# Kernel optimization log

Hardware: AMD Instinct MI355X
Metric: run time of the kernel (lower is better)

Reference implementation:

```python
import jax, jax.numpy as jnp
import numpy as np

NODE_DIM = 128
EDGE_ATTR_DIM = 64
OUT_DIM = 128
N_NODES = 10000
N_EDGES = 640000


def setup_inputs() -> dict:
    key = jax.random.key(0)
    k1, k2, k3, k4, k5, k6, k7 = jax.random.split(key, 7)
    x = jax.random.normal(k1, (N_NODES, NODE_DIM), dtype=jnp.float32)
    edge_index = jax.random.randint(k2, (2, N_EDGES), 0, N_NODES, dtype=jnp.int64)
    edge_attr = jax.random.normal(k3, (N_EDGES, EDGE_ATTR_DIM), dtype=jnp.float32)
    in_dim = 2 * NODE_DIM + EDGE_ATTR_DIM  # 320
    s1 = 1.0 / np.sqrt(in_dim)
    s2 = 1.0 / np.sqrt(OUT_DIM)
    W1 = jax.random.uniform(k4, (in_dim, OUT_DIM), jnp.float32, -s1, s1)
    b1 = jax.random.uniform(k5, (OUT_DIM,), jnp.float32, -s1, s1)
    W2 = jax.random.uniform(k6, (OUT_DIM, OUT_DIM), jnp.float32, -s2, s2)
    b2 = jax.random.uniform(k7, (OUT_DIM,), jnp.float32, -s2, s2)
    return {"x": x, "edge_index": edge_index, "edge_attr": edge_attr,
            "W1": W1, "b1": b1, "W2": W2, "b2": b2}


def reference(x, edge_index, edge_attr, W1, b1, W2, b2):
    src, tgt = edge_index[0], edge_index[1]
    x_i = x[src]                      # [E, node_dim] gather
    x_j = x[tgt]                      # [E, node_dim] gather
    edge_input = jnp.concatenate([x_i, x_j, edge_attr], axis=1)  # [E, 320]
    h = jax.nn.relu(edge_input @ W1 + b1)   # [E, out_dim]
    return h @ W2 + b2                      # [E, out_dim]
```

## Files before the change

### kernel.cpp

```cpp
#include <hip/hip_runtime.h>


typedef __bf16 bf16;
typedef __attribute__((ext_vector_type(8)))  __bf16 bf16x8;
typedef __attribute__((ext_vector_type(4)))  __bf16 bf16x4;
typedef __attribute__((ext_vector_type(16))) float  f32x16;

#define N_EDGES 640000
#define BM      256
#define NTHR    512

__global__ void prep_weights(const float* __restrict__ W1, const float* __restrict__ W2,
                             bf16* __restrict__ w1f, bf16* __restrict__ w2f) {
    int i = blockIdx.x * 256 + threadIdx.x;
    if (i < 40960) {
        int j = i & 7, l = (i >> 3) & 63, q = i >> 9;
        int ks = q % 20, nt = q / 20;
        int n = nt * 32 + (l & 31);
        int k = ks * 16 + ((l >> 5) << 3) + j;
        w1f[i] = (bf16)W1[k * 128 + n];
    } else if (i < 40960 + 16384) {
        int i2 = i - 40960;
        int j = i2 & 7, l = (i2 >> 3) & 63, q = i2 >> 9;
        int ks = q & 7, nt = q >> 3;
        int n = nt * 32 + (l & 31);
        int k = ks * 16 + ((l >> 5) << 3) + j;
        w2f[i2] = (bf16)W2[k * 128 + n];
    }
}

__device__ __forceinline__ void write_h(const f32x16& a, int mt, int nt, int ln, int rowq,
                                        bf16* sA, const float* sB1) {
    const int n    = nt * 32 + ln;
    const float bi = sB1[n];
    const int base = ((mt * 8 + (n >> 4)) * 64 + ((n >> 3) & 1) * 32) * 8 + (n & 7);
#pragma unroll
    for (int r = 0; r < 16; ++r) {
        const int ml = (r & 3) + ((r >> 2) << 3) + rowq;
        float v = a[r] + bi;
        sA[base + ml * 8] = (bf16)fmaxf(v, 0.f);
    }
}

__device__ __forceinline__ void write_out(const f32x16& a, int mt, int nt, int ln, int rowq,
                                          int ebase, const float* sB2, float* out) {
    const int n    = nt * 32 + ln;
    const float bi = sB2[n];
#pragma unroll
    for (int r = 0; r < 16; ++r) {
        const int ml = (r & 3) + ((r >> 2) << 3) + rowq;
        const size_t off = (size_t)(ebase + mt * 32 + ml) * 128 + n;
        __builtin_nontemporal_store(a[r] + bi, &out[off]);
    }
}

#define G1_STEP(KL, KS) {                                                          \
    bf16x8 a0  = *(const bf16x8*)&sA[((mt0 * 8 + (KL)) * 64 + lane) * 8];          \
    bf16x8 a1  = *(const bf16x8*)&sA[(((mt0 + 1) * 8 + (KL)) * 64 + lane) * 8];    \
    bf16x8 bb0 = *(const bf16x8*)&sW[((nt0 * 20 + (KS)) * 64 + lane) * 8];         \
    bf16x8 bb1 = *(const bf16x8*)&sW[(((nt0 + 1) * 20 + (KS)) * 64 + lane) * 8];   \
    acc00 = __builtin_amdgcn_mfma_f32_32x32x16_bf16(a0, bb0, acc00, 0, 0, 0);      \
    acc01 = __builtin_amdgcn_mfma_f32_32x32x16_bf16(a0, bb1, acc01, 0, 0, 0);      \
    acc10 = __builtin_amdgcn_mfma_f32_32x32x16_bf16(a1, bb0, acc10, 0, 0, 0);      \
    acc11 = __builtin_amdgcn_mfma_f32_32x32x16_bf16(a1, bb1, acc11, 0, 0, 0); }

#define G2_STEP(KS) {                                                              \
    bf16x8 a0  = *(const bf16x8*)&sA[((mt0 * 8 + (KS)) * 64 + lane) * 8];          \
    bf16x8 a1  = *(const bf16x8*)&sA[(((mt0 + 1) * 8 + (KS)) * 64 + lane) * 8];    \
    bf16x8 bb0 = *(const bf16x8*)&sW[((nt0 * 8 + (KS)) * 64 + lane) * 8];          \
    bf16x8 bb1 = *(const bf16x8*)&sW[(((nt0 + 1) * 8 + (KS)) * 64 + lane) * 8];    \
    acc00 = __builtin_amdgcn_mfma_f32_32x32x16_bf16(a0, bb0, acc00, 0, 0, 0);      \
    acc01 = __builtin_amdgcn_mfma_f32_32x32x16_bf16(a0, bb1, acc01, 0, 0, 0);      \
    acc10 = __builtin_amdgcn_mfma_f32_32x32x16_bf16(a1, bb0, acc10, 0, 0, 0);      \
    acc11 = __builtin_amdgcn_mfma_f32_32x32x16_bf16(a1, bb1, acc11, 0, 0, 0); }

__global__ __launch_bounds__(NTHR, 2) void edge_mlp(
    const float* __restrict__ x, const int* __restrict__ eidx,
    const float* __restrict__ eattr, const bf16* __restrict__ w1f,
    const float* __restrict__ b1, const bf16* __restrict__ w2f,
    const float* __restrict__ b2, float* __restrict__ out)
{
    extern __shared__ char smem[];
    bf16*  sW   = (bf16*)smem;
    bf16*  sA   = (bf16*)(smem + 81920);
    int*   sSrc = (int*)(smem + 81920 + 65536);
    int*   sTgt = sSrc + 256;
    float* sB1  = (float*)(sTgt + 256);
    float* sB2  = sB1 + 128;

    const int tid   = threadIdx.x;
    const int wave  = tid >> 6;
    const int lane  = tid & 63;
    const int ebase = blockIdx.x * BM;

    if (tid < BM) sSrc[tid] = eidx[ebase + tid];
    else          sTgt[tid - BM] = eidx[N_EDGES + ebase + (tid - BM)];
    if (tid < 128)        sB1[tid] = b1[tid];
    if (tid >= NTHR - 128) sB2[tid - (NTHR - 128)] = b2[tid - (NTHR - 128)];
    {
        const uint4* s4 = (const uint4*)w1f;
        uint4*       d4 = (uint4*)sW;
#pragma unroll
        for (int i = 0; i < 10; ++i) d4[i * NTHR + tid] = s4[i * NTHR + tid];
    }

    const int mt0 = (wave >> 1) * 2;
    const int nt0 = (wave & 1) * 2;

    f32x16 acc00, acc01, acc10, acc11;
#pragma unroll
    for (int i = 0; i < 16; ++i) { acc00[i] = 0.f; acc01[i] = 0.f; acc10[i] = 0.f; acc11[i] = 0.f; }

    const int m_st   = tid >> 1;
    const int ch     = (tid & 1) << 6;
    const int mt8_st = (m_st >> 5) * 8;
    const int ml_st  = m_st & 31;

#pragma unroll
    for (int p = 0; p < 2; ++p) {
        __syncthreads();
        {
            const int row = (p == 0) ? sSrc[m_st] : sTgt[m_st];
            const float4* xr = (const float4*)(x + (size_t)row * 128);
#pragma unroll
            for (int i = 0; i < 16; ++i) {
                const int c = ch + i * 4;
                float4 v = xr[c >> 2];
                bf16x4 bv; bv[0] = (bf16)v.x; bv[1] = (bf16)v.y; bv[2] = (bf16)v.z; bv[3] = (bf16)v.w;
                *((bf16x4*)&sA[((mt8_st + (c >> 4)) * 64 + ml_st + ((c >> 3) & 1) * 32) * 8 + (c & 7)]) = bv;
            }
        }
        __syncthreads();
#pragma unroll
        for (int kl = 0; kl < 8; ++kl) G1_STEP(kl, p * 8 + kl);
    }

    __syncthreads();
    {
#pragma unroll
        for (int i = 0; i < 8; ++i) {
            const int p4 = tid + i * NTHR;
            const int m  = p4 >> 4;
            const int c  = (p4 & 15) << 2;
            float4 v = ((const float4*)eattr)[(size_t)(ebase + m) * 16 + (p4 & 15)];
            bf16x4 bv; bv[0] = (bf16)v.x; bv[1] = (bf16)v.y; bv[2] = (bf16)v.z; bv[3] = (bf16)v.w;
            *((bf16x4*)&sA[(((m >> 5) * 8 + (c >> 4)) * 64 + (m & 31) + ((c >> 3) & 1) * 32) * 8 + (c & 7)]) = bv;
        }
    }
    __syncthreads();
#pragma unroll
    for (int kl = 0; kl < 4; ++kl) G1_STEP(kl, 16 + kl);

    __syncthreads();
    {
        const uint4* s4 = (const uint4*)w2f;
        uint4*       d4 = (uint4*)sW;
#pragma unroll
        for (int i = 0; i < 4; ++i) d4[i * NTHR + tid] = s4[i * NTHR + tid];
    }
    {
        const int rowq = (lane >> 5) * 4;
        const int ln   = lane & 31;
        write_h(acc00, mt0,     nt0,     ln, rowq, sA, sB1);
        write_h(acc01, mt0,     nt0 + 1, ln, rowq, sA, sB1);
        write_h(acc10, mt0 + 1, nt0,     ln, rowq, sA, sB1);
        write_h(acc11, mt0 + 1, nt0 + 1, ln, rowq, sA, sB1);
    }
    __syncthreads();

#pragma unroll
    for (int i = 0; i < 16; ++i) { acc00[i] = 0.f; acc01[i] = 0.f; acc10[i] = 0.f; acc11[i] = 0.f; }
#pragma unroll
    for (int ks = 0; ks < 8; ++ks) G2_STEP(ks);

    {
        const int rowq = (lane >> 5) * 4;
        const int ln   = lane & 31;
        write_out(acc00, mt0,     nt0,     ln, rowq, ebase, sB2, out);
        write_out(acc01, mt0,     nt0 + 1, ln, rowq, ebase, sB2, out);
        write_out(acc10, mt0 + 1, nt0,     ln, rowq, ebase, sB2, out);
        write_out(acc11, mt0 + 1, nt0 + 1, ln, rowq, ebase, sB2, out);
    }
}

extern "C" void kernel_launch(void* const* d_in, const int* in_sizes, int n_in,
                              void* d_out, int out_size, void* d_ws, size_t ws_size,
                              hipStream_t stream) {
    const float* x   = (const float*)d_in[0];
    const int*   ei  = (const int*)d_in[1];
    const float* ea  = (const float*)d_in[2];
    const float* W1  = (const float*)d_in[3];
    const float* b1  = (const float*)d_in[4];
    const float* W2  = (const float*)d_in[5];
    const float* b2  = (const float*)d_in[6];
    float*       out = (float*)d_out;

    bf16* w1f = (bf16*)d_ws;
    bf16* w2f = (bf16*)((char*)d_ws + 81920);

    prep_weights<<<224, 256, 0, stream>>>(W1, W2, w1f, w2f);

    const size_t shmem = 150528;
    edge_mlp<<<N_EDGES / BM, NTHR, shmem, stream>>>(x, ei, ea, w1f, b1, w2f, b2, out);
}
```

Measured before the change: 576.8 us.

## Shrink edge tile, keep weights in registers, swizzle hidden-layer LDS

Cuts the block tile from 256 to 64 edges with 256 threads, so LDS use drops from about 147KB to 56KB and more blocks fit per CU. Each wave now loads its own W1/W2 column slice straight into registers instead of staging the full weights in LDS, and the whole 320-wide gathered input is staged in one pass with no intermediate barriers. The hidden activations go to a separate XOR-swizzled LDS buffer to avoid bank conflicts, and setprio is raised around the MFMA loops. The cost is that every block reloads the weights from global memory/L2 (four times as many blocks) and holds more registers per thread.

After: 620.6 us. 7.6% more time.

```diff
diff --git a/kernel.cpp b/kernel.cpp
--- a/kernel.cpp
+++ b/kernel.cpp
@@ -3,12 +3,12 @@
 
 typedef __bf16 bf16;
 typedef __attribute__((ext_vector_type(8)))  __bf16 bf16x8;
-typedef __attribute__((ext_vector_type(4)))  __bf16 bf16x4;
+typedef __attribute__((ext_vector_type(4)))  float  f32x4;
 typedef __attribute__((ext_vector_type(16))) float  f32x16;
 
 #define N_EDGES 640000
-#define BM      256
-#define NTHR    512
+#define BM      64
+#define NTHR    256
 
 __global__ void prep_weights(const float* __restrict__ W1, const float* __restrict__ W2,
                              bf16* __restrict__ w1f, bf16* __restrict__ w2f) {
@@ -29,51 +29,6 @@
     }
 }
 
-__device__ __forceinline__ void write_h(const f32x16& a, int mt, int nt, int ln, int rowq,
-                                        bf16* sA, const float* sB1) {
-    const int n    = nt * 32 + ln;
-    const float bi = sB1[n];
-    const int base = ((mt * 8 + (n >> 4)) * 64 + ((n >> 3) & 1) * 32) * 8 + (n & 7);
-#pragma unroll
-    for (int r = 0; r < 16; ++r) {
-        const int ml = (r & 3) + ((r >> 2) << 3) + rowq;
-        float v = a[r] + bi;
-        sA[base + ml * 8] = (bf16)fmaxf(v, 0.f);
-    }
-}
-
-__device__ __forceinline__ void write_out(const f32x16& a, int mt, int nt, int ln, int rowq,
-                                          int ebase, const float* sB2, float* out) {
-    const int n    = nt * 32 + ln;
-    const float bi = sB2[n];
-#pragma unroll
-    for (int r = 0; r < 16; ++r) {
-        const int ml = (r & 3) + ((r >> 2) << 3) + rowq;
-        const size_t off = (size_t)(ebase + mt * 32 + ml) * 128 + n;
-        __builtin_nontemporal_store(a[r] + bi, &out[off]);
-    }
-}
-
-#define G1_STEP(KL, KS) {                                                          \
-    bf16x8 a0  = *(const bf16x8*)&sA[((mt0 * 8 + (KL)) * 64 + lane) * 8];          \
-    bf16x8 a1  = *(const bf16x8*)&sA[(((mt0 + 1) * 8 + (KL)) * 64 + lane) * 8];    \
-    bf16x8 bb0 = *(const bf16x8*)&sW[((nt0 * 20 + (KS)) * 64 + lane) * 8];         \
-    bf16x8 bb1 = *(const bf16x8*)&sW[(((nt0 + 1) * 20 + (KS)) * 64 + lane) * 8];   \
-    acc00 = __builtin_amdgcn_mfma_f32_32x32x16_bf16(a0, bb0, acc00, 0, 0, 0);      \
-    acc01 = __builtin_amdgcn_mfma_f32_32x32x16_bf16(a0, bb1, acc01, 0, 0, 0);      \
-    acc10 = __builtin_amdgcn_mfma_f32_32x32x16_bf16(a1, bb0, acc10, 0, 0, 0);      \
-    acc11 = __builtin_amdgcn_mfma_f32_32x32x16_bf16(a1, bb1, acc11, 0, 0, 0); }
-
-#define G2_STEP(KS) {                                                              \
-    bf16x8 a0  = *(const bf16x8*)&sA[((mt0 * 8 + (KS)) * 64 + lane) * 8];          \
-    bf16x8 a1  = *(const bf16x8*)&sA[(((mt0 + 1) * 8 + (KS)) * 64 + lane) * 8];    \
-    bf16x8 bb0 = *(const bf16x8*)&sW[((nt0 * 8 + (KS)) * 64 + lane) * 8];          \
-    bf16x8 bb1 = *(const bf16x8*)&sW[(((nt0 + 1) * 8 + (KS)) * 64 + lane) * 8];    \
-    acc00 = __builtin_amdgcn_mfma_f32_32x32x16_bf16(a0, bb0, acc00, 0, 0, 0);      \
-    acc01 = __builtin_amdgcn_mfma_f32_32x32x16_bf16(a0, bb1, acc01, 0, 0, 0);      \
-    acc10 = __builtin_amdgcn_mfma_f32_32x32x16_bf16(a1, bb0, acc10, 0, 0, 0);      \
-    acc11 = __builtin_amdgcn_mfma_f32_32x32x16_bf16(a1, bb1, acc11, 0, 0, 0); }
-
 __global__ __launch_bounds__(NTHR, 2) void edge_mlp(
     const float* __restrict__ x, const int* __restrict__ eidx,
     const float* __restrict__ eattr, const bf16* __restrict__ w1f,
@@ -81,105 +36,115 @@
     const float* __restrict__ b2, float* __restrict__ out)
 {
     extern __shared__ char smem[];
-    bf16*  sW   = (bf16*)smem;
-    bf16*  sA   = (bf16*)(smem + 81920);
-    int*   sSrc = (int*)(smem + 81920 + 65536);
-    int*   sTgt = sSrc + 256;
-    float* sB1  = (float*)(sTgt + 256);
-    float* sB2  = sB1 + 128;
+    bf16* sA = (bf16*)smem;
+    char* sH = smem + 40960;
 
     const int tid   = threadIdx.x;
     const int wave  = tid >> 6;
     const int lane  = tid & 63;
     const int ebase = blockIdx.x * BM;
 
-    if (tid < BM) sSrc[tid] = eidx[ebase + tid];
-    else          sTgt[tid - BM] = eidx[N_EDGES + ebase + (tid - BM)];
-    if (tid < 128)        sB1[tid] = b1[tid];
-    if (tid >= NTHR - 128) sB2[tid - (NTHR - 128)] = b2[tid - (NTHR - 128)];
-    {
-        const uint4* s4 = (const uint4*)w1f;
-        uint4*       d4 = (uint4*)sW;
 #pragma unroll
-        for (int i = 0; i < 10; ++i) d4[i * NTHR + tid] = s4[i * NTHR + tid];
+    for (int i = 0; i < 10; ++i) {
+        const int slot = i * NTHR + tid;
+        const int blk  = slot >> 6;
+        const int sub  = slot & 63;
+        const int mt   = blk / 20;
+        const int ks   = blk % 20;
+        const int m    = mt * 32 + (sub & 31);
+        const int k    = ks * 16 + ((sub >> 5) << 3);
+        f32x4 v0, v1;
+        if (ks < 8) {
+            const f32x4* p = (const f32x4*)(x + (size_t)eidx[ebase + m] * 128 + k);
+            v0 = p[0]; v1 = p[1];
+        } else if (ks < 16) {
+            const f32x4* p = (const f32x4*)(x + (size_t)eidx[N_EDGES + ebase + m] * 128 + (k - 128));
+            v0 = p[0]; v1 = p[1];
+        } else {
+            const f32x4* p = (const f32x4*)(eattr + (size_t)(ebase + m) * 64 + (k - 256));
+            v0 = __builtin_nontemporal_load(p);
+            v1 = __builtin_nontemporal_load(p + 1);
+        }
+        bf16x8 bv;
+        bv[0] = (bf16)v0.x; bv[1] = (bf16)v0.y; bv[2] = (bf16)v0.z; bv[3] = (bf16)v0.w;
+        bv[4] = (bf16)v1.x; bv[5] = (bf16)v1.y; bv[6] = (bf16)v1.z; bv[7] = (bf16)v1.w;
+        *(bf16x8*)&sA[slot * 8] = bv;
     }
 
-    const int mt0 = (wave >> 1) * 2;
-    const int nt0 = (wave & 1) * 2;
-
-    f32x16 acc00, acc01, acc10, acc11;
+    bf16x8 w1r[20];
+    {
+        const bf16x8* wp = (const bf16x8*)w1f + (wave * 20 * 64 + lane);
 #pragma unroll
-    for (int i = 0; i < 16; ++i) { acc00[i] = 0.f; acc01[i] = 0.f; acc10[i] = 0.f; acc11[i] = 0.f; }
-
-    const int m_st   = tid >> 1;
-    const int ch     = (tid & 1) << 6;
-    const int mt8_st = (m_st >> 5) * 8;
-    const int ml_st  = m_st & 31;
-
-#pragma unroll
-    for (int p = 0; p < 2; ++p) {
-        __syncthreads();
-        {
-            const int row = (p == 0) ? sSrc[m_st] : sTgt[m_st];
-            const float4* xr = (const float4*)(x + (size_t)row * 128);
-#pragma unroll
-            for (int i = 0; i < 16; ++i) {
-                const int c = ch + i * 4;
-                float4 v = xr[c >> 2];
-                bf16x4 bv; bv[0] = (bf16)v.x; bv[1] = (bf16)v.y; bv[2] = (bf16)v.z; bv[3] = (bf16)v.w;
-                *((bf16x4*)&sA[((mt8_st + (c >> 4)) * 64 + ml_st + ((c >> 3) & 1) * 32) * 8 + (c & 7)]) = bv;
-            }
-        }
-        __syncthreads();
-#pragma unroll
-        for (int kl = 0; kl < 8; ++kl) G1_STEP(kl, p * 8 + kl);
+        for (int ks = 0; ks < 20; ++ks) w1r[ks] = wp[ks * 64];
     }
 
-    __syncthreads();
-    {
+    f32x16 acc0, acc1;
 #pragma unroll
-        for (int i = 0; i < 8; ++i) {
-            const int p4 = tid + i * NTHR;
-            const int m  = p4 >> 4;
-            const int c  = (p4 & 15) << 2;
-            float4 v = ((const float4*)eattr)[(size_t)(ebase + m) * 16 + (p4 & 15)];
-            bf16x4 bv; bv[0] = (bf16)v.x; bv[1] = (bf16)v.y; bv[2] = (bf16)v.z; bv[3] = (bf16)v.w;
-            *((bf16x4*)&sA[(((m >> 5) * 8 + (c >> 4)) * 64 + (m & 31) + ((c >> 3) & 1) * 32) * 8 + (c & 7)]) = bv;
-        }
-    }
-    __syncthreads();
-#pragma unroll
-    for (int kl = 0; kl < 4; ++kl) G1_STEP(kl, 16 + kl);
+    for (int i = 0; i < 16; ++i) { acc0[i] = 0.f; acc1[i] = 0.f; }
 
     __syncthreads();
+
+    __builtin_amdgcn_s_setprio(1);
+#pragma unroll
+    for (int ks = 0; ks < 20; ++ks) {
+        bf16x8 a0 = *(const bf16x8*)&sA[((0 * 20 + ks) * 64 + lane) * 8];
+        bf16x8 a1 = *(const bf16x8*)&sA[((1 * 20 + ks) * 64 + lane) * 8];
+        acc0 = __builtin_amdgcn_mfma_f32_32x32x16_bf16(a0, w1r[ks], acc0, 0, 0, 0);
+        acc1 = __builtin_amdgcn_mfma_f32_32x32x16_bf16(a1, w1r[ks], acc1, 0, 0, 0);
+    }
+    __builtin_amdgcn_s_setprio(0);
+
+    bf16x8 w2r[8];
     {
-        const uint4* s4 = (const uint4*)w2f;
-        uint4*       d4 = (uint4*)sW;
+        const bf16x8* wp = (const bf16x8*)w2f + (wave * 8 * 64 + lane);
 #pragma unroll
-        for (int i = 0; i < 4; ++i) d4[i * NTHR + tid] = s4[i * NTHR + tid];
+        for (int ks = 0; ks < 8; ++ks) w2r[ks] = wp[ks * 64];
     }
+
     {
-        const int rowq = (lane >> 5) * 4;
-        const int ln   = lane & 31;
-        write_h(acc00, mt0,     nt0,     ln, rowq, sA, sB1);
-        write_h(acc01, mt0,     nt0 + 1, ln, rowq, sA, sB1);
-        write_h(acc10, mt0 + 1, nt0,     ln, rowq, sA, sB1);
-        write_h(acc11, mt0 + 1, nt0 + 1, ln, rowq, sA, sB1);
+        const int   ln   = lane & 31;
+        const int   kn   = wave * 32 + ln;
+        const int   rowq = (lane >> 5) << 2;
+        const float b1v  = b1[kn];
+        const int   colb = ((kn >> 4) * 64 + ((kn >> 3) & 1) * 32) * 16 + (kn & 7) * 2;
+        const int   kx   = ((kn >> 3) & 7) << 5;
+#pragma unroll
+        for (int r = 0; r < 16; ++r) {
+            const int ml  = (r & 3) + ((r >> 2) << 3) + rowq;
+            const int off = colb + ml * 16;
+            *(bf16*)(sH + ((off       ) ^ kx)) = (bf16)fmaxf(acc0[r] + b1v, 0.f);
+            *(bf16*)(sH + ((off + 8192) ^ kx)) = (bf16)fmaxf(acc1[r] + b1v, 0.f);
+        }
     }
     __syncthreads();
 
 #pragma unroll
-    for (int i = 0; i < 16; ++i) { acc00[i] = 0.f; acc01[i] = 0.f; acc10[i] = 0.f; acc11[i] = 0.f; }
+    for (int i = 0; i < 16; ++i) { acc0[i] = 0.f; acc1[i] = 0.f; }
+    __builtin_amdgcn_s_setprio(1);
 #pragma unroll
-    for (int ks = 0; ks < 8; ++ks) G2_STEP(ks);
+    for (int ks = 0; ks < 8; ++ks) {
+        int o0 = ((0 * 8 + ks) * 64 + lane) * 16;
+        int o1 = ((1 * 8 + ks) * 64 + lane) * 16;
+        o0 ^= ((o0 >> 9) & 7) << 5;
+        o1 ^= ((o1 >> 9) & 7) << 5;
+        bf16x8 a0 = *(const bf16x8*)(sH + o0);
+        bf16x8 a1 = *(const bf16x8*)(sH + o1);
+        acc0 = __builtin_amdgcn_mfma_f32_32x32x16_bf16(a0, w2r[ks], acc0, 0, 0, 0);
+        acc1 = __builtin_amdgcn_mfma_f32_32x32x16_bf16(a1, w2r[ks], acc1, 0, 0, 0);
+    }
+    __builtin_amdgcn_s_setprio(0);
 
     {
-        const int rowq = (lane >> 5) * 4;
-        const int ln   = lane & 31;
-        write_out(acc00, mt0,     nt0,     ln, rowq, ebase, sB2, out);
-        write_out(acc01, mt0,     nt0 + 1, ln, rowq, ebase, sB2, out);
-        write_out(acc10, mt0 + 1, nt0,     ln, rowq, ebase, sB2, out);
-        write_out(acc11, mt0 + 1, nt0 + 1, ln, rowq, ebase, sB2, out);
+        const int   ln   = lane & 31;
+        const int   n    = wave * 32 + ln;
+        const int   rowq = (lane >> 5) << 2;
+        const float b2v  = b2[n];
+#pragma unroll
+        for (int r = 0; r < 16; ++r) {
+            const int ml = (r & 3) + ((r >> 2) << 3) + rowq;
+            __builtin_nontemporal_store(acc0[r] + b2v, &out[(size_t)(ebase      + ml) * 128 + n]);
+            __builtin_nontemporal_store(acc1[r] + b2v, &out[(size_t)(ebase + 32 + ml) * 128 + n]);
+        }
     }
 }
 
@@ -200,6 +165,6 @@
 
     prep_weights<<<224, 256, 0, stream>>>(W1, W2, w1f, w2f);
 
-    const size_t shmem = 150528;
+    const size_t shmem = 40960 + 16384;
     edge_mlp<<<N_EDGES / BM, NTHR, shmem, stream>>>(x, ei, ea, w1f, b1, w2f, b2, out);
 }
```
